# Performance work log

Measured on AMD Instinct MI355X. Metric: run time of the kernel, lower is better.

Reference implementation:

```python
import jax, jax.numpy as jnp
import numpy as np


def setup_inputs() -> dict:
    key = jax.random.key(0)
    k1, k2 = jax.random.split(key)
    B, N, M, D = 8, 8192, 8192, 3
    input1 = jax.random.normal(k1, (B, N, D), dtype=jnp.float32)
    input2 = jax.random.normal(k2, (B, M, D), dtype=jnp.float32)
    return {"input1": input1, "input2": input2}


def reference(input1, input2):
    # input1: [B, N, 3], input2: [B, M, 3]
    # Squared pairwise distances via ||x||^2 + ||y||^2 - 2<x,y>
    sq1 = jnp.sum(input1 * input1, axis=-1)          # [B, N]
    sq2 = jnp.sum(input2 * input2, axis=-1)          # [B, M]
    inner = jnp.einsum('bnd,bmd->bnm', input1, input2)  # [B, N, M]
    d = sq1[:, :, None] + sq2[:, None, :] - 2.0 * inner  # [B, N, M]
    d = jnp.maximum(d, 0.0)  # numerical guard
    dist1 = jnp.min(d, axis=2)  # [B, N] NN in input2 for each point of input1
    dist2 = jnp.min(d, axis=1)  # [B, M] NN in input1 for each point of input2
    loss = jnp.mean(dist1) + jnp.mean(dist2)
    return loss
```

## Files before the change

### kernel.cpp

```cpp
#include <hip/hip_runtime.h>


typedef _Float16 half8 __attribute__((ext_vector_type(8)));
typedef float    f16x  __attribute__((ext_vector_type(16)));

constexpr int B       = 8;
constexpr int NPTS    = 8192;
constexpr int TOTAL   = B * NPTS;
constexpr int NSTRIP  = 256;
constexpr int NSTRIPS = NPTS / NSTRIP;
constexpr int MH      = 2;
constexpr int MHALF   = NPTS / MH;
constexpr int CHUNK   = 512;
constexpr int NWAVE   = 8;

__device__ __forceinline__ float colmin16(const f16x& a)
{
    float m0 = fminf(fminf(a[0],  a[1]),  a[2]);
    float m1 = fminf(fminf(a[3],  a[4]),  a[5]);
    float m2 = fminf(fminf(a[6],  a[7]),  a[8]);
    float m3 = fminf(fminf(a[9],  a[10]), a[11]);
    float m4 = fminf(fminf(a[12], a[13]), a[14]);
    return fminf(fminf(fminf(m0, m1), m2), fminf(fminf(m3, m4), a[15]));
}

__global__ __launch_bounds__(512, 4) void chamfer_mfma(
    const float* __restrict__ in1, const float* __restrict__ in2,
    float* __restrict__ d1p, float* __restrict__ d2p, float* __restrict__ out)
{
    const int b     = blockIdx.z;
    const int strip = blockIdx.x;
    const int mh    = blockIdx.y;
    const int wave  = threadIdx.x >> 6;
    const int lane  = threadIdx.x & 63;
    const int col   = lane & 31;
    const int half  = lane >> 5;

    if ((blockIdx.x | blockIdx.y | blockIdx.z) == 0 && threadIdx.x == 0)
        *out = 0.0f;

    __shared__ _Float16 ldsB[CHUNK * 16];
    __shared__ float    d2w[NWAVE][CHUNK];

    const int nbase = strip * NSTRIP + wave * 32;
    half8 afrag;
    {
        const float* a = in1 + ((size_t)b * NPTS + nbase + col) * 3;
        float x = a[0], y = a[1], z = a[2];
        float sq = fmaf(x, x, fmaf(y, y, z * z));
        _Float16 xh = (_Float16)x, yh = (_Float16)y, zh = (_Float16)z;
        _Float16 xl = (_Float16)(x - (float)xh);
        _Float16 yl = (_Float16)(y - (float)yh);
        _Float16 zl = (_Float16)(z - (float)zh);
        _Float16 sh = (_Float16)sq, sl = (_Float16)(sq - (float)sh);
        half8 lo = {xh, yh, zh, xl, yl, zl, xh, yh};
        half8 hi = {zh, sh, sl, (_Float16)1.f, (_Float16)1.f,
                    (_Float16)0.f, (_Float16)0.f, (_Float16)0.f};
        afrag = half ? hi : lo;
    }

    f16x MN1, zacc;
#pragma unroll
    for (int r = 0; r < 16; ++r) { MN1[r] = 1e30f; zacc[r] = 0.0f; }

    const float* Craw = in2 + ((size_t)b * NPTS + mh * MHALF) * 3;
    float* d2 = d2p + ((size_t)b * NSTRIPS + strip) * NPTS + mh * MHALF;

    for (int c = 0; c < MHALF / CHUNK; ++c) {
        __syncthreads();
        {
            const int i = threadIdx.x;
            const float* cp = Craw + (size_t)(c * CHUNK + i) * 3;
            float cx = cp[0], cy = cp[1], cz = cp[2];
            float x = -2.f * cx, y = -2.f * cy, z = -2.f * cz;
            float sq = fmaf(cx, cx, fmaf(cy, cy, cz * cz));
            _Float16 xh = (_Float16)x, yh = (_Float16)y, zh = (_Float16)z;
            _Float16 xl = (_Float16)(x - (float)xh);
            _Float16 yl = (_Float16)(y - (float)yh);
            _Float16 zl = (_Float16)(z - (float)zh);
            _Float16 sh = (_Float16)sq, sl = (_Float16)(sq - (float)sh);
            half8 lo = {xh, yh, zh, xh, yh, zh, xl, yl};
            half8 hi = {zl, (_Float16)1.f, (_Float16)1.f, sh, sl,
                        (_Float16)0.f, (_Float16)0.f, (_Float16)0.f};
            *(half8*)&ldsB[(i >> 5) * 512 + (i & 31) * 8]       = lo;
            *(half8*)&ldsB[(i >> 5) * 512 + 256 + (i & 31) * 8] = hi;
        }
        if (c > 0) {
            const int i = threadIdx.x;
            float v = d2w[0][i];
#pragma unroll
            for (int w = 1; w < NWAVE; ++w) v = fminf(v, d2w[w][i]);
            d2[(c - 1) * CHUNK + i] = fmaxf(v, 0.0f);
        }
        __syncthreads();

#pragma unroll 2
        for (int t = 0; t < CHUNK / 32; t += 2) {
            half8 bfA = *(const half8*)&ldsB[ t      * 512 + lane * 8];
            half8 bfB = *(const half8*)&ldsB[(t + 1) * 512 + lane * 8];
            f16x accA = __builtin_amdgcn_mfma_f32_32x32x16_f16(afrag, bfA, zacc, 0, 0, 0);
            f16x accB = __builtin_amdgcn_mfma_f32_32x32x16_f16(afrag, bfB, zacc, 0, 0, 0);

#pragma unroll
            for (int r = 0; r < 16; ++r)
                MN1[r] = fminf(fminf(accA[r], accB[r]), MN1[r]);

            float vA = colmin16(accA);
            float vB = colmin16(accB);
            vA = fminf(vA, __shfl_xor(vA, 32, 64));
            vB = fminf(vB, __shfl_xor(vB, 32, 64));
            d2w[wave][(t + half) * 32 + col] = half ? vB : vA;
        }
    }
    __syncthreads();
    {
        const int i = threadIdx.x;
        float v = d2w[0][i];
#pragma unroll
        for (int w = 1; w < NWAVE; ++w) v = fminf(v, d2w[w][i]);
        d2[(MHALF / CHUNK - 1) * CHUNK + i] = fmaxf(v, 0.0f);
    }

#pragma unroll
    for (int m = 1; m <= 16; m <<= 1)
#pragma unroll
        for (int r = 0; r < 16; ++r)
            MN1[r] = fminf(MN1[r], __shfl_xor(MN1[r], m, 64));
    if (col == 0) {
        float* d1 = d1p + ((size_t)b * MH + mh) * NPTS + nbase;
#pragma unroll
        for (int r = 0; r < 16; ++r)
            d1[(r & 3) + 8 * (r >> 2) + 4 * half] = MN1[r];
    }
}

__global__ __launch_bounds__(64) void reduce_kernel(
    const float* __restrict__ d1p, const float* __restrict__ d2p,
    float* __restrict__ out)
{
    int g  = blockIdx.x * 64 + threadIdx.x;
    int b  = g >> 11;
    int mq = g & 2047;

    const float4* p2 = (const float4*)(d2p + (size_t)b * NSTRIPS * NPTS) + mq;
    float4 v2 = p2[0];
#pragma unroll 8
    for (int s = 1; s < NSTRIPS; ++s) {
        float4 t = p2[(size_t)s * (NPTS / 4)];
        v2.x = fminf(v2.x, t.x); v2.y = fminf(v2.y, t.y);
        v2.z = fminf(v2.z, t.z); v2.w = fminf(v2.w, t.w);
    }
    const float4* p1 = (const float4*)(d1p + (size_t)b * MH * NPTS) + mq;
    float4 a = p1[0];
#pragma unroll
    for (int s = 1; s < MH; ++s) {
        float4 t = p1[(size_t)s * (NPTS / 4)];
        a.x = fminf(a.x, t.x); a.y = fminf(a.y, t.y);
        a.z = fminf(a.z, t.z); a.w = fminf(a.w, t.w);
    }
    float v = fmaxf(a.x, 0.0f) + fmaxf(a.y, 0.0f)
            + fmaxf(a.z, 0.0f) + fmaxf(a.w, 0.0f)
            + v2.x + v2.y + v2.z + v2.w;

#pragma unroll
    for (int off = 32; off; off >>= 1)
        v += __shfl_down(v, off, 64);
    if (threadIdx.x == 0)
        atomicAdd(out, v * (1.0f / (float)TOTAL));
}

extern "C" void kernel_launch(void* const* d_in, const int* in_sizes, int n_in,
                              void* d_out, int out_size, void* d_ws, size_t ws_size,
                              hipStream_t stream)
{
    const float* in1 = (const float*)d_in[0];
    const float* in2 = (const float*)d_in[1];
    float* out = (float*)d_out;

    char* ws = (char*)d_ws;
    float* d1p = (float*)ws;
    float* d2p = (float*)(ws + (size_t)MH * TOTAL * 4);

    chamfer_mfma<<<dim3(NSTRIPS, MH, B), 512, 0, stream>>>(
        in1, in2, d1p, d2p, out);
    reduce_kernel<<<TOTAL / 4 / 64, 64, 0, stream>>>(d1p, d2p, out);
}
```

Before: 97.45 us.

## Prefetch next chunk of input2 into registers and split M into quarters

The next chunk's input2 coordinates are now loaded into registers during the current chunk's MFMA loop, so global load latency is hidden behind compute instead of sitting between the two barriers. MH goes from 2 to 4, doubling the grid so more blocks can run concurrently. The launch-bounds occupancy hint goes from 4 to 8 blocks. The trade-off is more partial d1 outputs for the reduce kernel and tighter register limits, which could cause spills.

Measured after the change: 100.9 us. +3.5%, slower.

```diff
diff --git a/kernel.cpp b/kernel.cpp
--- a/kernel.cpp
+++ b/kernel.cpp
@@ -9,9 +9,10 @@
 constexpr int TOTAL   = B * NPTS;
 constexpr int NSTRIP  = 256;
 constexpr int NSTRIPS = NPTS / NSTRIP;
-constexpr int MH      = 2;
+constexpr int MH      = 4;
 constexpr int MHALF   = NPTS / MH;
 constexpr int CHUNK   = 512;
+constexpr int NCHUNK  = MHALF / CHUNK;
 constexpr int NWAVE   = 8;
 
 __device__ __forceinline__ float colmin16(const f16x& a)
@@ -24,7 +25,7 @@
     return fminf(fminf(fminf(m0, m1), m2), fminf(fminf(m3, m4), a[15]));
 }
 
-__global__ __launch_bounds__(512, 4) void chamfer_mfma(
+__global__ __launch_bounds__(512, 8) void chamfer_mfma(
     const float* __restrict__ in1, const float* __restrict__ in2,
     float* __restrict__ d1p, float* __restrict__ d2p, float* __restrict__ out)
 {
@@ -66,31 +67,38 @@
     const float* Craw = in2 + ((size_t)b * NPTS + mh * MHALF) * 3;
     float* d2 = d2p + ((size_t)b * NSTRIPS + strip) * NPTS + mh * MHALF;
 
-    for (int c = 0; c < MHALF / CHUNK; ++c) {
-        __syncthreads();
+    float px, py, pz;
+    {
+        const float* cp = Craw + (size_t)threadIdx.x * 3;
+        px = cp[0]; py = cp[1]; pz = cp[2];
+    }
+
+    for (int c = 0; c < NCHUNK; ++c) {
+        half8 plo, phi;
         {
-            const int i = threadIdx.x;
-            const float* cp = Craw + (size_t)(c * CHUNK + i) * 3;
-            float cx = cp[0], cy = cp[1], cz = cp[2];
-            float x = -2.f * cx, y = -2.f * cy, z = -2.f * cz;
-            float sq = fmaf(cx, cx, fmaf(cy, cy, cz * cz));
+            float x = -2.f * px, y = -2.f * py, z = -2.f * pz;
+            float sq = fmaf(px, px, fmaf(py, py, pz * pz));
             _Float16 xh = (_Float16)x, yh = (_Float16)y, zh = (_Float16)z;
             _Float16 xl = (_Float16)(x - (float)xh);
             _Float16 yl = (_Float16)(y - (float)yh);
             _Float16 zl = (_Float16)(z - (float)zh);
             _Float16 sh = (_Float16)sq, sl = (_Float16)(sq - (float)sh);
-            half8 lo = {xh, yh, zh, xh, yh, zh, xl, yl};
-            half8 hi = {zl, (_Float16)1.f, (_Float16)1.f, sh, sl,
+            plo = half8{xh, yh, zh, xh, yh, zh, xl, yl};
+            phi = half8{zl, (_Float16)1.f, (_Float16)1.f, sh, sl,
                         (_Float16)0.f, (_Float16)0.f, (_Float16)0.f};
-            *(half8*)&ldsB[(i >> 5) * 512 + (i & 31) * 8]       = lo;
-            *(half8*)&ldsB[(i >> 5) * 512 + 256 + (i & 31) * 8] = hi;
         }
+        __syncthreads();
+        *(half8*)&ldsB[(threadIdx.x >> 5) * 512 + (threadIdx.x & 31) * 8]       = plo;
+        *(half8*)&ldsB[(threadIdx.x >> 5) * 512 + 256 + (threadIdx.x & 31) * 8] = phi;
         if (c > 0) {
-            const int i = threadIdx.x;
-            float v = d2w[0][i];
+            float v = d2w[0][threadIdx.x];
 #pragma unroll
-            for (int w = 1; w < NWAVE; ++w) v = fminf(v, d2w[w][i]);
-            d2[(c - 1) * CHUNK + i] = fmaxf(v, 0.0f);
+            for (int w = 1; w < NWAVE; ++w) v = fminf(v, d2w[w][threadIdx.x]);
+            d2[(c - 1) * CHUNK + threadIdx.x] = fmaxf(v, 0.0f);
+        }
+        if (c + 1 < NCHUNK) {
+            const float* cp = Craw + (size_t)((c + 1) * CHUNK + threadIdx.x) * 3;
+            px = cp[0]; py = cp[1]; pz = cp[2];
         }
         __syncthreads();
 
@@ -114,11 +122,10 @@
     }
     __syncthreads();
     {
-        const int i = threadIdx.x;
-        float v = d2w[0][i];
+        float v = d2w[0][threadIdx.x];
 #pragma unroll
-        for (int w = 1; w < NWAVE; ++w) v = fminf(v, d2w[w][i]);
-        d2[(MHALF / CHUNK - 1) * CHUNK + i] = fmaxf(v, 0.0f);
+        for (int w = 1; w < NWAVE; ++w) v = fminf(v, d2w[w][threadIdx.x]);
+        d2[(NCHUNK - 1) * CHUNK + threadIdx.x] = fmaxf(v, 0.0f);
     }
 
 #pragma unroll
```
